# Kernel tuning notes

Hardware: AMD Instinct MI355X
Metric: run time of the kernel (lower is better)

The kernel has to match this reference:

```python
import jax, jax.numpy as jnp
import numpy as np

# ---- static configuration (from init_kwargs) ----
L = 36.0            # cubic cell edge (bohr)
G = 180             # grid points per axis
NA = 64             # number of atoms
NRAD = 8            # basis['n']
NL = 4              # basis['l']
RO = 2.5            # basis['r_o'] (bohr)
A = L / G           # grid spacing (orthorhombic -> U = diag(A))
RMAX = int(np.ceil(RO / A))          # half-width of periodic box (13)
B = 2 * RMAX + 1                     # box edge (27)
VCELL = A ** 3                       # |det U|
# static coefficient mask: keep (n,l,m) with |m - NL| <= l  (same as tril*flip(tril))
_MASK = np.abs(np.arange(2 * NL + 1)[None, :] - NL) <= np.arange(NL)[:, None]


def _make_W():
    # orthonormalization matrix W = S^{-1/2} for radials phi_n(r) = r^2 (r_o - r)^{n+2}
    r = np.linspace(0.0, RO, 4000)
    phi = np.stack([r ** 2 * (RO - r) ** (n + 2) for n in range(NRAD)])
    S = np.trapz(phi[:, None] * phi[None, :], r, axis=-1)
    w, v = np.linalg.eigh(S)
    return (v @ np.diag(w ** -0.5) @ v.T).astype(np.float32)


def setup_inputs() -> dict:
    key = jax.random.key(0)
    k1, k2 = jax.random.split(key)
    rho = jax.random.uniform(k1, (G, G, G), dtype=jnp.float32)       # electron density >= 0
    positions = jax.random.uniform(k2, (NA, 3), dtype=jnp.float32) * L
    return {"rho": rho, "positions": positions, "W": jnp.asarray(_make_W())}


def _sph_padded(theta, phi):
    # real spherical harmonics, zero-padded to [NL, 2*NL+1, ...] with m at index NL+m
    ct = jnp.cos(theta); st = jnp.sin(theta)
    cp = jnp.cos(phi); sp = jnp.sin(phi)
    c2p = jnp.cos(2 * phi); s2p = jnp.sin(2 * phi)
    c3p = jnp.cos(3 * phi); s3p = jnp.sin(3 * phi)
    z = jnp.zeros_like(theta)
    one = jnp.ones_like(theta)
    Y = {
        (0, 0): 0.28209479177387814 * one,
        (1, -1): 0.4886025119029199 * st * sp,
        (1, 0): 0.4886025119029199 * ct,
        (1, 1): 0.4886025119029199 * st * cp,
        (2, -2): 0.5462742152960396 * st ** 2 * s2p,
        (2, -1): 1.0925484305920792 * st * ct * sp,
        (2, 0): 0.31539156525252005 * (3 * ct ** 2 - 1),
        (2, 1): 1.0925484305920792 * st * ct * cp,
        (2, 2): 0.5462742152960396 * st ** 2 * c2p,
        (3, -3): 0.5900435899266435 * st ** 3 * s3p,
        (3, -2): 1.445305721320277 * st ** 2 * ct * s2p,
        (3, -1): 0.4570457994644658 * st * (5 * ct ** 2 - 1) * sp,
        (3, 0): 0.3731763325901154 * (5 * ct ** 3 - 3 * ct),
        (3, 1): 0.4570457994644658 * st * (5 * ct ** 2 - 1) * cp,
        (3, 2): 1.445305721320277 * st ** 2 * ct * c2p,
        (3, 3): 0.5900435899266435 * st ** 3 * c3p,
    }
    rows = []
    for l in range(NL):
        pad = [z] * (NL - l)
        rows.append(jnp.stack(pad + [Y[(l, m)] for m in range(-l, l + 1)] + pad))
    return jnp.stack(rows)  # [NL, 2NL+1, B, B, B]


def _project_atom(rho, pos, W):
    a = jnp.float32(A)
    cm = jnp.round(pos / a)            # nearest grid index of atom (U_inv @ pos)
    dr = pos - a * cm                  # sub-grid displacement
    offs = jnp.arange(-RMAX, RMAX + 1, dtype=jnp.float32)
    # periodic mesh indices (box_around / fmod wrap)
    Xm = jnp.mod(offs + cm[0], G).astype(jnp.int32)
    Ym = jnp.mod(offs + cm[1], G).astype(jnp.int32)
    Zm = jnp.mod(offs + cm[2], G).astype(jnp.int32)
    srho = rho[Xm[:, None, None], Ym[None, :, None], Zm[None, None, :]]  # [B,B,B] gather
    # euclidean coords relative to the atom
    Xs = (offs * a - dr[0])[:, None, None]
    Ys = (offs * a - dr[1])[None, :, None]
    Zs = (offs * a - dr[2])[None, None, :]
    Xs, Ys, Zs = jnp.broadcast_arrays(Xs, Ys, Zs)
    R = jnp.sqrt(Xs ** 2 + Ys ** 2 + Zs ** 2)
    Rsafe = jnp.where(R < 1e-12, 1.0, R)
    Theta = jnp.where(R < 1e-12, 0.0, jnp.arccos(jnp.clip(Zs / Rsafe, -1.0, 1.0)))
    Phi = jnp.arctan2(Ys, Xs)
    angs = _sph_padded(Theta, Phi)                       # [NL, 2NL+1, B,B,B]
    ns = jnp.arange(NRAD, dtype=jnp.float32)[:, None, None, None]
    phi_n = jnp.where(R < RO, R ** 2 * jnp.maximum(RO - R, 0.0) ** (ns + 2.0), 0.0)
    rads = jnp.einsum('nm,mijk->nijk', W, phi_n) * jnp.float32(VCELL)  # [NRAD, B,B,B]
    coeff = jnp.einsum('lmijk,nijk,ijk->nlm', angs, rads, srho)        # [NRAD, NL, 2NL+1]
    return coeff[:, _MASK].reshape(-1)                    # [NRAD * NL^2] = 128


def reference(rho, positions, W):
    # vmap over atoms (single species -> identical box shape per atom)
    return jax.vmap(lambda p: _project_atom(rho, p, W))(positions)  # [NA, 128]
```

## Files before the change

kernel.cpp:

```cpp
#include <hip/hip_runtime.h>

#define G 180
#define NRAD 8
#define RO_F 2.5f
#define A_F 0.2f
#define VCELL_F 0.008f
#define CELLS 19683
#define SLABS 16
#define NATOMS 64
#define ITERS 10


__global__ __launch_bounds__(256, 3) void proj_kernel(
    const float* __restrict__ rho, const float* __restrict__ pos,
    float* __restrict__ ws)
{
    const int atom = blockIdx.y;
    const int slab = blockIdx.x;
    const int tid  = threadIdx.x;
    const int lane = tid & 63;
    const int w    = tid >> 6;
    const int g    = w >> 1;
    const int cw   = w & 1;

    const float px = pos[atom*3+0], py = pos[atom*3+1], pz = pos[atom*3+2];
    const float cmx = rintf(px * 5.0f), cmy = rintf(py * 5.0f), cmz = rintf(pz * 5.0f);
    const float drx = px - A_F*cmx, dry = py - A_F*cmy, drz = pz - A_F*cmz;
    const int icx = (int)cmx - 13, icy = (int)cmy - 13, icz = (int)cmz - 13;

    float acc[64];
    #pragma unroll
    for (int j = 0; j < 64; ++j) acc[j] = 0.0f;

    int c = slab*128 + cw*64 + lane;

    int i_n, j_n, k_n; float s_n;
    {
        int i = c / 729; int rem = c - i*729; int j = rem / 27; int k = rem - j*27;
        int gx = i + icx; gx += (gx < 0) ? G : 0; gx -= (gx >= G) ? G : 0;
        int gy = j + icy; gy += (gy < 0) ? G : 0; gy -= (gy >= G) ? G : 0;
        int gz = k + icz; gz += (gz < 0) ? G : 0; gz -= (gz >= G) ? G : 0;
        i_n = i; j_n = j; k_n = k;
        s_n = rho[(gx*G + gy)*G + gz];
    }

    for (int it = 0; it < ITERS; ++it) {
        const int i = i_n, j = j_n, k = k_n;
        const float s = s_n;
        c += SLABS*128;
        if (it != ITERS-1) {
            int i2 = c / 729; int rem = c - i2*729; int j2 = rem / 27; int k2 = rem - j2*27;
            int gx = i2 + icx; gx += (gx < 0) ? G : 0; gx -= (gx >= G) ? G : 0;
            int gy = j2 + icy; gy += (gy < 0) ? G : 0; gy -= (gy >= G) ? G : 0;
            int gz = k2 + icz; gz += (gz < 0) ? G : 0; gz -= (gz >= G) ? G : 0;
            i_n = i2; j_n = j2; k_n = k2;
            s_n = rho[(gx*G + gy)*G + gz];
        }

        float x = (float)(i-13)*A_F - drx;
        float y = (float)(j-13)*A_F - dry;
        float z = (float)(k-13)*A_F - drz;
        float r2 = x*x + y*y + z*z;
        float inv = rsqrtf(fmaxf(r2, 1e-24f));
        float R = r2 * inv;
        if (R < RO_F) {
            float t = RO_F - R;
            float ux = x*inv, uy = y*inv, uz = z*inv;
            float uz2 = uz*uz;
            float ux2 = ux*ux, uy2 = uy*uy;
            float ys[16];
            ys[0]  = 0.28209479177f;
            ys[1]  = 0.48860251190f * uy;
            ys[2]  = 0.48860251190f * uz;
            ys[3]  = 0.48860251190f * ux;
            ys[4]  = 1.09254843059f * ux*uy;
            ys[5]  = 1.09254843059f * uy*uz;
            ys[6]  = 0.31539156525f * (3.0f*uz2 - 1.0f);
            ys[7]  = 1.09254843059f * ux*uz;
            ys[8]  = 0.54627421530f * (ux2 - uy2);
            ys[9]  = 0.59004358993f * uy*(3.0f*ux2 - uy2);
            ys[10] = 2.89061144264f * ux*uy*uz;
            ys[11] = 0.45704579946f * uy*(5.0f*uz2 - 1.0f);
            ys[12] = 0.37317633259f * uz*(5.0f*uz2 - 3.0f);
            ys[13] = 0.45704579946f * ux*(5.0f*uz2 - 1.0f);
            ys[14] = 1.44530572132f * (ux2 - uy2)*uz;
            ys[15] = 0.59004358993f * ux*(ux2 - 3.0f*uy2);

            float t2 = t*t;
            float p0 = s * r2 * t2;
            if (g) { float t4 = t2*t2; p0 *= t4; }
            float p1 = p0*t, p2 = p1*t, p3 = p2*t;
            #pragma unroll
            for (int q = 0; q < 16; ++q) {
                acc[q]    = fmaf(p0, ys[q], acc[q]);
                acc[16+q] = fmaf(p1, ys[q], acc[16+q]);
                acc[32+q] = fmaf(p2, ys[q], acc[32+q]);
                acc[48+q] = fmaf(p3, ys[q], acc[48+q]);
            }
        }
    }

    __shared__ float red[4][64][33];
    __shared__ float stage[4][2][32];
    const int col  = lane & 31;
    const int half = lane >> 5;
    #pragma unroll
    for (int ch = 0; ch < 2; ++ch) {
        #pragma unroll
        for (int q = 0; q < 32; ++q)
            red[w][lane][q] = acc[ch*32 + q];
        float csum = 0.0f;
        #pragma unroll
        for (int r = 0; r < 32; ++r)
            csum += red[w][half*32 + r][col];
        stage[w][half][col] = csum;
        if (lane < 32) {
            float v = stage[w][0][lane] + stage[w][1][lane];
            ws[((atom*SLABS + slab)*4 + w)*64 + ch*32 + lane] = v;
        }
    }
}

__global__ void finalize_kernel(const float* __restrict__ ws,
                                const float* __restrict__ W,
                                float* __restrict__ out)
{
    const int atom = blockIdx.x;
    const int t = threadIdx.x;
    const int n = t >> 4, q = t & 15;
    const int g = n >> 2, r = n & 3;
    const float* base = ws + atom*SLABS*4*64;
    float m = 0.0f;
    #pragma unroll
    for (int s = 0; s < SLABS; ++s) {
        m += base[(s*4 + g*2 + 0)*64 + r*16 + q];
        m += base[(s*4 + g*2 + 1)*64 + r*16 + q];
    }
    __shared__ float M[8][16];
    M[n][q] = m;
    __syncthreads();
    float sum = 0.0f;
    #pragma unroll
    for (int k = 0; k < 8; ++k)
        sum = fmaf(W[n*8+k], M[k][q], sum);
    out[atom*128 + t] = sum * VCELL_F;
}

extern "C" void kernel_launch(void* const* d_in, const int* in_sizes, int n_in,
                              void* d_out, int out_size, void* d_ws, size_t ws_size,
                              hipStream_t stream) {
    const float* rho = (const float*)d_in[0];
    const float* pos = (const float*)d_in[1];
    const float* W   = (const float*)d_in[2];
    float* out = (float*)d_out;
    float* ws  = (float*)d_ws;

    dim3 grid(SLABS, NATOMS);
    proj_kernel<<<grid, 256, 0, stream>>>(rho, pos, ws);
    finalize_kernel<<<NATOMS, 128, 0, stream>>>(ws, W, out);
}
```

Measured before the change: 80.23 us.

## Fuse finalize into projection kernel using per-atom completion flags

Removes the separate finalize launch. Each block publishes its partial sums and sets a flag, and block slab 0 of each atom spin-waits on all 16 flags before doing the W contraction and writing the output. It then resets the flags for the next call. This saves a kernel launch and its gap, but it relies on the other slabs being co-resident or scheduled ahead (a deadlock risk), depends on the workspace flags starting at zero, and lowers launch_bounds occupancy to 2. The stage smem buffer is also replaced by a cross-lane shuffle.

```diff
diff --git a/kernel.cpp b/kernel.cpp
--- a/kernel.cpp
+++ b/kernel.cpp
@@ -9,10 +9,14 @@
 #define SLABS 16
 #define NATOMS 64
 #define ITERS 10
+#define MAGIC 0x1ACEB00Cu
+
+#define FLAG_OFF (NATOMS * SLABS * 4 * 64)
 
 
-__global__ __launch_bounds__(256, 3) void proj_kernel(
+__global__ __launch_bounds__(256, 2) void proj_fused_kernel(
     const float* __restrict__ rho, const float* __restrict__ pos,
+    const float* __restrict__ W, float* __restrict__ out,
     float* __restrict__ ws)
 {
     const int atom = blockIdx.y;
@@ -101,7 +105,6 @@
     }
 
     __shared__ float red[4][64][33];
-    __shared__ float stage[4][2][32];
     const int col  = lane & 31;
     const int half = lane >> 5;
     #pragma unroll
@@ -113,37 +116,51 @@
         #pragma unroll
         for (int r = 0; r < 32; ++r)
             csum += red[w][half*32 + r][col];
-        stage[w][half][col] = csum;
-        if (lane < 32) {
-            float v = stage[w][0][lane] + stage[w][1][lane];
-            ws[((atom*SLABS + slab)*4 + w)*64 + ch*32 + lane] = v;
+        float other = __shfl_down(csum, 32);
+        if (lane < 32)
+            ws[((atom*SLABS + slab)*4 + w)*64 + ch*32 + lane] = csum + other;
+    }
+
+    unsigned* flags = (unsigned*)(ws + FLAG_OFF);
+    __threadfence();
+    __syncthreads();
+    if (tid == 0)
+        atomicExch(&flags[atom*SLABS + slab], MAGIC);
+
+    if (slab == 0) {
+        if (tid < SLABS) {
+            while (__hip_atomic_load(&flags[atom*SLABS + tid],
+                                     __ATOMIC_RELAXED,
+                                     __HIP_MEMORY_SCOPE_AGENT) != MAGIC) {}
         }
+        __syncthreads();
+        __threadfence();
+        if (tid < 128) {
+            const int n = tid >> 4, q = tid & 15;
+            const int gg = n >> 2, r = n & 3;
+            const float* base = ws + atom*SLABS*4*64;
+            float m = 0.0f;
+            #pragma unroll
+            for (int s = 0; s < SLABS; ++s) {
+                m += base[(s*4 + gg*2 + 0)*64 + r*16 + q];
+                m += base[(s*4 + gg*2 + 1)*64 + r*16 + q];
+            }
+            __shared__ float M[8][16];
+            M[n][q] = m;
+            __syncthreads();
+            float sum = 0.0f;
+            #pragma unroll
+            for (int k = 0; k < 8; ++k)
+                sum = fmaf(W[n*8+k], M[k][q], sum);
+            out[atom*128 + tid] = sum * VCELL_F;
+        } else {
+            __syncthreads();
+        }
+        __syncthreads();
+        if (tid < SLABS)
+            __hip_atomic_store(&flags[atom*SLABS + tid], 0u,
+                               __ATOMIC_RELAXED, __HIP_MEMORY_SCOPE_AGENT);
     }
-}
-
-__global__ void finalize_kernel(const float* __restrict__ ws,
-                                const float* __restrict__ W,
-                                float* __restrict__ out)
-{
-    const int atom = blockIdx.x;
-    const int t = threadIdx.x;
-    const int n = t >> 4, q = t & 15;
-    const int g = n >> 2, r = n & 3;
-    const float* base = ws + atom*SLABS*4*64;
-    float m = 0.0f;
-    #pragma unroll
-    for (int s = 0; s < SLABS; ++s) {
-        m += base[(s*4 + g*2 + 0)*64 + r*16 + q];
-        m += base[(s*4 + g*2 + 1)*64 + r*16 + q];
-    }
-    __shared__ float M[8][16];
-    M[n][q] = m;
-    __syncthreads();
-    float sum = 0.0f;
-    #pragma unroll
-    for (int k = 0; k < 8; ++k)
-        sum = fmaf(W[n*8+k], M[k][q], sum);
-    out[atom*128 + t] = sum * VCELL_F;
 }
 
 extern "C" void kernel_launch(void* const* d_in, const int* in_sizes, int n_in,
@@ -156,6 +173,5 @@
     float* ws  = (float*)d_ws;
 
     dim3 grid(SLABS, NATOMS);
-    proj_kernel<<<grid, 256, 0, stream>>>(rho, pos, ws);
-    finalize_kernel<<<NATOMS, 128, 0, stream>>>(ws, W, out);
+    proj_fused_kernel<<<grid, 256, 0, stream>>>(rho, pos, W, out, ws);
 }
```

After: 191.5 us. 2.39x slower.
